# Optimization experiments

Hardware: AMD Instinct MI355X
Metric: run time of the kernel (lower is better)

The kernel has to match this reference:

```python
import jax, jax.numpy as jnp
import numpy as np

N = 100000
E = 3200000
D = 128


def spmm(row, col, val, x, n):
    # y[i] = sum_{e: row[e]==i} val[e] * x[col[e]]  -- COO SpMM via gather + segment_sum
    msgs = x[col] * val[:, None]          # [E, D]
    return jax.ops.segment_sum(msgs, row, num_segments=n)


def setup_inputs() -> dict:
    key = jax.random.key(0)
    ks = jax.random.split(key, 8)
    edge_row = jnp.sort(jax.random.randint(ks[0], (E,), 0, N))
    edge_col = jax.random.randint(ks[1], (E,), 0, N)
    edge_val = jax.random.uniform(ks[2], (E,), dtype=jnp.float32) / 32.0  # ~normalized laplacian weights
    selfloop_diag = jnp.ones((N,), dtype=jnp.float32)
    features = jax.random.normal(ks[3], (N, D), dtype=jnp.float32)
    W1 = jax.random.normal(ks[4], (D, D), dtype=jnp.float32) * 0.05
    b1 = jax.random.normal(ks[5], (D,), dtype=jnp.float32) * 0.05
    W2 = jax.random.normal(ks[6], (D, D), dtype=jnp.float32) * 0.05
    b2 = jax.random.normal(ks[7], (D,), dtype=jnp.float32) * 0.05
    return {"edge_row": edge_row, "edge_col": edge_col, "edge_val": edge_val,
            "selfloop_diag": selfloop_diag, "features": features,
            "W1": W1, "b1": b1, "W2": W2, "b2": b2}


def reference(edge_row, edge_col, edge_val, selfloop_diag, features, W1, b1, W2, b2):
    n = features.shape[0]
    Lx = spmm(edge_row, edge_col, edge_val, features, n)       # L @ features
    inter_feats = Lx * features                                 # elementwise mul
    L1x = Lx + selfloop_diag[:, None] * features                 # (L + I) @ features
    part1 = L1x @ W1.T + b1                                      # linear1
    part2 = spmm(edge_row, edge_col, edge_val, inter_feats, n) @ W2.T + b2  # linear2(L @ inter)
    return part1 + part2
```

## Files before the change

kernel.cpp:

```cpp
#include <hip/hip_runtime.h>

#define DD 128

typedef unsigned int uint32;
typedef unsigned short ushort_t;
typedef __attribute__((ext_vector_type(8))) short short8;
typedef __attribute__((ext_vector_type(4))) float f32x4;
typedef __attribute__((ext_vector_type(2))) float f32x2;

__device__ __forceinline__ uint32 pack_bf16(float a, float b) {
    uint32 ua = __builtin_bit_cast(uint32, a);
    uint32 ub = __builtin_bit_cast(uint32, b);
    ua = (ua + 0x7fffu + ((ua >> 16) & 1u)) >> 16;
    ub = (ub + 0x7fffu + ((ub >> 16) & 1u)) >> 16;
    return ua | (ub << 16);
}

#if __has_builtin(__builtin_amdgcn_cvt_pk_f32_fp8) && __has_builtin(__builtin_amdgcn_cvt_pk_fp8_f32)
#define FP8_HW 1
#else
#define FP8_HW 0
#endif

#if !FP8_HW
__device__ __forceinline__ float fp8_dec1(uint32 b) {
    uint32 s = (b >> 7) & 1, e = (b >> 3) & 15, m = b & 7;
    float v = (e == 0) ? ldexpf((float)m, -9) : ldexpf((float)(8 + m), (int)e - 10);
    return s ? -v : v;
}
__device__ __forceinline__ uint32 fp8_enc1(float x) {
    uint32 u = __builtin_bit_cast(uint32, x);
    uint32 s = (u >> 31) << 7;
    float ax = fabsf(x);
    if (ax >= 448.f) return s | 0x7E;
    if (ax < 0.0009765625f) return s;
    if (ax >= 0.015625f) {
        uint32 e = (u >> 23) & 0xFF;
        uint32 m = u & 0x7FFFFF;
        uint32 keep = m >> 20, rest = m & 0xFFFFF;
        keep += (rest > 0x80000u) || (rest == 0x80000u && (keep & 1));
        uint32 ee = e - 127 + 7;
        if (keep == 8) { keep = 0; ee += 1; }
        if (ee > 15 || (ee == 15 && keep > 6)) return s | 0x7E;
        return s | (ee << 3) | keep;
    }
    uint32 ni = (uint32)(ax * 512.f + 0.5f);
    if (ni >= 8) return s | (1u << 3);
    return s | ni;
}
#endif

template <bool WORD>
__device__ __forceinline__ f32x2 fp8x2_dec(uint32 u) {
#if FP8_HW
    return __builtin_amdgcn_cvt_pk_f32_fp8(u, WORD);
#else
    uint32 v = WORD ? (u >> 16) : u;
    f32x2 r; r.x = fp8_dec1(v & 0xff); r.y = fp8_dec1((v >> 8) & 0xff);
    return r;
#endif
}

__device__ __forceinline__ uint32 fp8x2_enc(float a, float b) {
#if FP8_HW
    return __builtin_amdgcn_cvt_pk_fp8_f32(a, b, 0, false) & 0xffffu;
#else
    return fp8_enc1(a) | (fp8_enc1(b) << 8);
#endif
}

__device__ __forceinline__ uint32 fp8x4_enc(float4 f) {
#if FP8_HW
    uint32 w = __builtin_amdgcn_cvt_pk_fp8_f32(f.x, f.y, 0, false);
    w = __builtin_amdgcn_cvt_pk_fp8_f32(f.z, f.w, w, true);
    return w;
#else
    return fp8_enc1(f.x) | (fp8_enc1(f.y) << 8) | (fp8_enc1(f.z) << 16) | (fp8_enc1(f.w) << 24);
#endif
}

__global__ __launch_bounds__(256) void k_row_ptr(const int* __restrict__ row,
                                                 int* __restrict__ rp, int n, int e) {
    int i = blockIdx.x * 256 + threadIdx.x;
    if (i > n) return;
    int lo = 0, hi = e;
    while (lo < hi) { int m = (lo + hi) >> 1; if (row[m] < i) lo = m + 1; else hi = m; }
    rp[i] = lo;
}

__global__ __launch_bounds__(256) void k_prep(const float* __restrict__ feat,
                                              uint32* __restrict__ featq,
                                              const float* __restrict__ W1,
                                              const float* __restrict__ W2,
                                              uint32* __restrict__ Wb1,
                                              uint32* __restrict__ Wb2, int n) {
    int id = blockIdx.x * 256 + threadIdx.x;
    if (id < n * (DD / 4)) {
        float4 f = ((const float4*)feat)[id];
        featq[id] = fp8x4_enc(f);
    }
    if (id < 2 * DD * DD / 4) {
        int mat = id >> 12, rem = id & 4095;
        float4 wv = ((const float4*)(mat ? W2 : W1))[rem];
        uint2 p;
        p.x = pack_bf16(wv.x, wv.y);
        p.y = pack_bf16(wv.z, wv.w);
        ((uint2*)(mat ? Wb2 : Wb1))[rem] = p;
    }
}

template <int PASS>
__global__ __launch_bounds__(256) void k_spmm(const int* __restrict__ col,
                                              const float* __restrict__ val,
                                              const ushort_t* __restrict__ xq,
                                              const int* __restrict__ rp,
                                              const float* __restrict__ feat,
                                              const float* __restrict__ diag,
                                              uint32* __restrict__ out1,
                                              ushort_t* __restrict__ out2, int n) {
    int lane = threadIdx.x & 63;
    int row = blockIdx.x * 4 + (threadIdx.x >> 6);
    if (row >= n) return;
    row = __builtin_amdgcn_readfirstlane(row);
    int s = rp[row], eend = rp[row + 1];
    float ax = 0.f, ay = 0.f;
    int e = s;

#define SPMM_BATCH(UNN)                                                        \
    {                                                                          \
        int c[UNN]; float vv[UNN]; uint32 g[UNN];                              \
        _Pragma("unroll")                                                      \
        for (int u = 0; u < UNN; ++u) { c[u] = col[e + u]; vv[u] = val[e + u]; } \
        _Pragma("unroll")                                                      \
        for (int u = 0; u < UNN; ++u) { g[u] = xq[((size_t)c[u] << 6) + lane]; } \
        _Pragma("unroll")                                                      \
        for (int u = 0; u < UNN; ++u) {                                        \
            f32x2 d = fp8x2_dec<false>(g[u]);                                  \
            ax = fmaf(vv[u], d.x, ax);                                         \
            ay = fmaf(vv[u], d.y, ay);                                         \
        }                                                                      \
    }

    for (; e + 16 <= eend; e += 16) SPMM_BATCH(16)
    if (e + 8 <= eend) { SPMM_BATCH(8) e += 8; }
    if (e + 4 <= eend) { SPMM_BATCH(4) e += 4; }
    for (; e < eend; ++e) {
        int c = col[e]; float v = val[e];
        uint32 g = xq[((size_t)c << 6) + lane];
        f32x2 d = fp8x2_dec<false>(g);
        ax = fmaf(v, d.x, ax);
        ay = fmaf(v, d.y, ay);
    }
#undef SPMM_BATCH

    if (PASS == 1) {
        float dg = diag[row];
        float2 f = ((const float2*)feat)[(size_t)row * 64 + lane];
        out1[(size_t)row * 64 + lane] = pack_bf16(fmaf(dg, f.x, ax), fmaf(dg, f.y, ay));
        out2[(size_t)row * 64 + lane] = (ushort_t)fp8x2_enc(ax * f.x, ay * f.y);
    } else {
        out1[(size_t)row * 64 + lane] = pack_bf16(ax, ay);
    }
}

__global__ __launch_bounds__(512, 2) void k_gemm(const uint32* __restrict__ Abf,
                                                 const uint32* __restrict__ Bbf,
                                                 const uint32* __restrict__ Wb1g,
                                                 const uint32* __restrict__ Wb2g,
                                                 const float* __restrict__ b1,
                                                 const float* __restrict__ b2,
                                                 float* __restrict__ out, int n) {
    __shared__ __align__(16) char lds[65536];
    int t = threadIdx.x;
    {
        const uint2* s1 = (const uint2*)Wb1g;
        const uint2* s2 = (const uint2*)Wb2g;
#pragma unroll
        for (int u = 0; u < 16; ++u) {
            int id = u * 512 + t;
            int j = id >> 5, kq = id & 31;
            int dst = j * 256 + ((kq * 8) ^ ((j & 7) << 4));
            *(uint2*)(lds + dst) = s1[id];
            *(uint2*)(lds + 32768 + dst) = s2[id];
        }
    }
    __syncthreads();
    int lane = t & 63, w = t >> 6;
    int g = lane >> 4;
    int rowbase = blockIdx.x * 256 + w * 32;
    int rr = rowbase + (lane & 15);
    int r0 = min(rr, n - 1);
    int r1 = min(rr + 16, n - 1);
    const uint4* A4 = (const uint4*)Abf;
    const uint4* B4 = (const uint4*)Bbf;

    f32x4 acc[2][8];
#pragma unroll
    for (int mt = 0; mt < 2; ++mt)
#pragma unroll
        for (int jt = 0; jt < 8; ++jt) acc[mt][jt] = (f32x4){0.f, 0.f, 0.f, 0.f};

    uint4 a0 = A4[(size_t)r0 * 16 + g], a1 = A4[(size_t)r1 * 16 + g];
    uint4 c0 = B4[(size_t)r0 * 16 + g], c1 = B4[(size_t)r1 * 16 + g];
#pragma unroll
    for (int kc = 0; kc < 4; ++kc) {
        uint4 na0, na1, nc0, nc1;
        if (kc < 3) {
            na0 = A4[(size_t)r0 * 16 + (kc + 1) * 4 + g];
            na1 = A4[(size_t)r1 * 16 + (kc + 1) * 4 + g];
            nc0 = B4[(size_t)r0 * 16 + (kc + 1) * 4 + g];
            nc1 = B4[(size_t)r1 * 16 + (kc + 1) * 4 + g];
        }
        short8 fa0 = __builtin_bit_cast(short8, a0);
        short8 fa1 = __builtin_bit_cast(short8, a1);
        short8 fc0 = __builtin_bit_cast(short8, c0);
        short8 fc1 = __builtin_bit_cast(short8, c1);
        int kbase = kc * 64 + g * 16;
#pragma unroll
        for (int jt = 0; jt < 8; ++jt) {
            int j = jt * 16 + (lane & 15);
            int off = j * 256 + (kbase ^ ((j & 7) << 4));
            short8 w1 = *(const short8*)(lds + off);
            short8 w2 = *(const short8*)(lds + 32768 + off);
            acc[0][jt] = __builtin_amdgcn_mfma_f32_16x16x32_bf16(fa0, w1, acc[0][jt], 0, 0, 0);
            acc[0][jt] = __builtin_amdgcn_mfma_f32_16x16x32_bf16(fc0, w2, acc[0][jt], 0, 0, 0);
            acc[1][jt] = __builtin_amdgcn_mfma_f32_16x16x32_bf16(fa1, w1, acc[1][jt], 0, 0, 0);
            acc[1][jt] = __builtin_amdgcn_mfma_f32_16x16x32_bf16(fc1, w2, acc[1][jt], 0, 0, 0);
        }
        a0 = na0; a1 = na1; c0 = nc0; c1 = nc1;
    }
    float bsum[8];
#pragma unroll
    for (int jt = 0; jt < 8; ++jt) {
        int cj = jt * 16 + (lane & 15);
        bsum[jt] = b1[cj] + b2[cj];
    }
#pragma unroll
    for (int mt = 0; mt < 2; ++mt) {
#pragma unroll
        for (int i = 0; i < 4; ++i) {
            int r = rowbase + mt * 16 + g * 4 + i;
            if (r < n) {
                float* orow = out + (size_t)r * DD;
#pragma unroll
                for (int jt = 0; jt < 8; ++jt)
                    orow[jt * 16 + (lane & 15)] = acc[mt][jt][i] + bsum[jt];
            }
        }
    }
}

extern "C" void kernel_launch(void* const* d_in, const int* in_sizes, int n_in,
                              void* d_out, int out_size, void* d_ws, size_t ws_size,
                              hipStream_t stream) {
    const int*   edge_row = (const int*)d_in[0];
    const int*   edge_col = (const int*)d_in[1];
    const float* edge_val = (const float*)d_in[2];
    const float* diag     = (const float*)d_in[3];
    const float* feat     = (const float*)d_in[4];
    const float* W1       = (const float*)d_in[5];
    const float* b1       = (const float*)d_in[6];
    const float* W2       = (const float*)d_in[7];
    const float* b2       = (const float*)d_in[8];
    float* out = (float*)d_out;

    const int E = in_sizes[0];
    const int N = in_sizes[3];

    char* ws = (char*)d_ws;
    size_t off = 0;
    int* rp            = (int*)(ws + off);      off += (((size_t)(N + 1) * 4) + 255) & ~(size_t)255;
    uint32* featq      = (uint32*)(ws + off);   off += (size_t)N * (DD / 4) * 4;
    uint32* interq     = (uint32*)(ws + off);   off += (size_t)N * (DD / 4) * 4;
    uint32* L1xbf      = (uint32*)(ws + off);   off += (size_t)N * (DD / 2) * 4;
    uint32* Linterbf   = (uint32*)(ws + off);   off += (size_t)N * (DD / 2) * 4;
    uint32* Wb1g       = (uint32*)(ws + off);   off += (size_t)DD * (DD / 2) * 4;
    uint32* Wb2g       = (uint32*)(ws + off);   off += (size_t)DD * (DD / 2) * 4;
    (void)ws_size; (void)n_in; (void)out_size;

    k_row_ptr<<<(N + 1 + 255) / 256, 256, 0, stream>>>(edge_row, rp, N, E);
    {
        int work = N * (DD / 4);
        if (work < 2 * DD * DD / 4) work = 2 * DD * DD / 4;
        k_prep<<<(work + 255) / 256, 256, 0, stream>>>(feat, featq, W1, W2, Wb1g, Wb2g, N);
    }
    k_spmm<1><<<(N + 3) / 4, 256, 0, stream>>>(edge_col, edge_val, (const ushort_t*)featq, rp,
                                               feat, diag, L1xbf, (ushort_t*)interq, N);
    k_spmm<2><<<(N + 3) / 4, 256, 0, stream>>>(edge_col, edge_val, (const ushort_t*)interq, rp,
                                               nullptr, nullptr, Linterbf, nullptr, N);
    k_gemm<<<(N + 255) / 256, 512, 0, stream>>>(L1xbf, Linterbf, Wb1g, Wb2g, b1, b2, out, N);
}
```

Before: 168.0 us.

## Split each wavefront into two half-waves processing alternate edges with 4-byte gathers

Each row's 64-lane wavefront now splits into two 32-lane halves. Each half handles alternate edges and gathers 4 fp8 features per lane as one 32-bit load instead of 2 features per 16-bit load. Partial sums from the two halves are combined with a cross-half shuffle, and only the low half writes wider outputs. This halves the number of gather instructions per row and improves per-load width, at the cost of the extra shuffle reduction, lane-select logic, and idle upper lanes during the epilogue.

```diff
diff --git a/kernel.cpp b/kernel.cpp
--- a/kernel.cpp
+++ b/kernel.cpp
@@ -3,7 +3,6 @@
 #define DD 128
 
 typedef unsigned int uint32;
-typedef unsigned short ushort_t;
 typedef __attribute__((ext_vector_type(8))) short short8;
 typedef __attribute__((ext_vector_type(4))) float f32x4;
 typedef __attribute__((ext_vector_type(2))) float f32x2;
@@ -61,14 +60,6 @@
 #endif
 }
 
-__device__ __forceinline__ uint32 fp8x2_enc(float a, float b) {
-#if FP8_HW
-    return __builtin_amdgcn_cvt_pk_fp8_f32(a, b, 0, false) & 0xffffu;
-#else
-    return fp8_enc1(a) | (fp8_enc1(b) << 8);
-#endif
-}
-
 __device__ __forceinline__ uint32 fp8x4_enc(float4 f) {
 #if FP8_HW
     uint32 w = __builtin_amdgcn_cvt_pk_fp8_f32(f.x, f.y, 0, false);
@@ -112,54 +103,75 @@
 template <int PASS>
 __global__ __launch_bounds__(256) void k_spmm(const int* __restrict__ col,
                                               const float* __restrict__ val,
-                                              const ushort_t* __restrict__ xq,
+                                              const uint32* __restrict__ xq,
                                               const int* __restrict__ rp,
                                               const float* __restrict__ feat,
                                               const float* __restrict__ diag,
-                                              uint32* __restrict__ out1,
-                                              ushort_t* __restrict__ out2, int n) {
+                                              uint2* __restrict__ out1,
+                                              uint32* __restrict__ out2, int n) {
     int lane = threadIdx.x & 63;
     int row = blockIdx.x * 4 + (threadIdx.x >> 6);
     if (row >= n) return;
     row = __builtin_amdgcn_readfirstlane(row);
     int s = rp[row], eend = rp[row + 1];
-    float ax = 0.f, ay = 0.f;
+    uint32 d32 = (uint32)(lane & 31);
+    bool hi = lane >= 32;
+    f32x2 a01 = {0.f, 0.f}, a23 = {0.f, 0.f};
     int e = s;
 
-#define SPMM_BATCH(UNN)                                                        \
+#define SPMM_B2(NE)                                                            \
     {                                                                          \
-        int c[UNN]; float vv[UNN]; uint32 g[UNN];                              \
+        int c[NE]; float v[NE];                                                \
         _Pragma("unroll")                                                      \
-        for (int u = 0; u < UNN; ++u) { c[u] = col[e + u]; vv[u] = val[e + u]; } \
+        for (int u = 0; u < NE; ++u) { c[u] = col[e + u]; v[u] = val[e + u]; } \
+        uint32 g[NE / 2]; float vs[NE / 2];                                    \
         _Pragma("unroll")                                                      \
-        for (int u = 0; u < UNN; ++u) { g[u] = xq[((size_t)c[u] << 6) + lane]; } \
+        for (int u = 0; u < NE / 2; ++u) {                                     \
+            int cs = hi ? c[2 * u + 1] : c[2 * u];                             \
+            g[u] = xq[((uint32)cs << 5) + d32];                                \
+            vs[u] = hi ? v[2 * u + 1] : v[2 * u];                              \
+        }                                                                      \
         _Pragma("unroll")                                                      \
-        for (int u = 0; u < UNN; ++u) {                                        \
-            f32x2 d = fp8x2_dec<false>(g[u]);                                  \
-            ax = fmaf(vv[u], d.x, ax);                                         \
-            ay = fmaf(vv[u], d.y, ay);                                         \
+        for (int u = 0; u < NE / 2; ++u) {                                     \
+            f32x2 w = {vs[u], vs[u]};                                          \
+            a01 += w * fp8x2_dec<false>(g[u]);                                 \
+            a23 += w * fp8x2_dec<true >(g[u]);                                 \
         }                                                                      \
     }
 
-    for (; e + 16 <= eend; e += 16) SPMM_BATCH(16)
-    if (e + 8 <= eend) { SPMM_BATCH(8) e += 8; }
-    if (e + 4 <= eend) { SPMM_BATCH(4) e += 4; }
-    for (; e < eend; ++e) {
-        int c = col[e]; float v = val[e];
-        uint32 g = xq[((size_t)c << 6) + lane];
-        f32x2 d = fp8x2_dec<false>(g);
-        ax = fmaf(v, d.x, ax);
-        ay = fmaf(v, d.y, ay);
-    }
-#undef SPMM_BATCH
-
-    if (PASS == 1) {
-        float dg = diag[row];
-        float2 f = ((const float2*)feat)[(size_t)row * 64 + lane];
-        out1[(size_t)row * 64 + lane] = pack_bf16(fmaf(dg, f.x, ax), fmaf(dg, f.y, ay));
-        out2[(size_t)row * 64 + lane] = (ushort_t)fp8x2_enc(ax * f.x, ay * f.y);
-    } else {
-        out1[(size_t)row * 64 + lane] = pack_bf16(ax, ay);
+    for (; e + 16 <= eend; e += 16) SPMM_B2(16)
+    if (e + 8 <= eend) { SPMM_B2(8) e += 8; }
+    if (e + 4 <= eend) { SPMM_B2(4) e += 4; }
+    if (e + 2 <= eend) { SPMM_B2(2) e += 2; }
+    if (e < eend) {
+        int c0 = col[e]; float v0 = val[e];
+        uint32 g = xq[((uint32)c0 << 5) + d32];
+        float vv = hi ? 0.f : v0;
+        f32x2 w = {vv, vv};
+        a01 += w * fp8x2_dec<false>(g);
+        a23 += w * fp8x2_dec<true >(g);
+    }
+#undef SPMM_B2
+
+    a01.x += __shfl_xor(a01.x, 32, 64); a01.y += __shfl_xor(a01.y, 32, 64);
+    a23.x += __shfl_xor(a23.x, 32, 64); a23.y += __shfl_xor(a23.y, 32, 64);
+
+    if (lane < 32) {
+        if (PASS == 1) {
+            float dg = diag[row];
+            float4 f = ((const float4*)feat)[(size_t)row * 32 + d32];
+            uint2 o;
+            o.x = pack_bf16(fmaf(dg, f.x, a01.x), fmaf(dg, f.y, a01.y));
+            o.y = pack_bf16(fmaf(dg, f.z, a23.x), fmaf(dg, f.w, a23.y));
+            out1[(size_t)row * 32 + d32] = o;
+            out2[(size_t)row * 32 + d32] =
+                fp8x4_enc(make_float4(a01.x * f.x, a01.y * f.y, a23.x * f.z, a23.y * f.w));
+        } else {
+            uint2 o;
+            o.x = pack_bf16(a01.x, a01.y);
+            o.y = pack_bf16(a23.x, a23.y);
+            out1[(size_t)row * 32 + d32] = o;
+        }
     }
 }
 
@@ -284,9 +296,9 @@
         if (work < 2 * DD * DD / 4) work = 2 * DD * DD / 4;
         k_prep<<<(work + 255) / 256, 256, 0, stream>>>(feat, featq, W1, W2, Wb1g, Wb2g, N);
     }
-    k_spmm<1><<<(N + 3) / 4, 256, 0, stream>>>(edge_col, edge_val, (const ushort_t*)featq, rp,
-                                               feat, diag, L1xbf, (ushort_t*)interq, N);
-    k_spmm<2><<<(N + 3) / 4, 256, 0, stream>>>(edge_col, edge_val, (const ushort_t*)interq, rp,
-                                               nullptr, nullptr, Linterbf, nullptr, N);
+    k_spmm<1><<<(N + 3) / 4, 256, 0, stream>>>(edge_col, edge_val, featq, rp,
+                                               feat, diag, (uint2*)L1xbf, interq, N);
+    k_spmm<2><<<(N + 3) / 4, 256, 0, stream>>>(edge_col, edge_val, interq, rp,
+                                               nullptr, nullptr, (uint2*)Linterbf, nullptr, N);
     k_gemm<<<(N + 255) / 256, 512, 0, stream>>>(L1xbf, Linterbf, Wb1g, Wb2g, b1, b2, out, N);
 }
```

New measurement: 164.6 us, median of 2. -2.0%, faster.
